# Kernel optimization log

Hardware: AMD Instinct MI355X
Metric: run time of the kernel (lower is better)

Reference implementation:

```python
import jax, jax.numpy as jnp
import numpy as np
from jax import lax

N_NODES = 10000
N_EDGES = 320000


def setup_inputs() -> dict:
    key = jax.random.key(0)
    ks = jax.random.split(key, 7)
    B, H, N, F = 4, 24, N_NODES, 32
    hid = 64
    x = jax.random.normal(ks[0], (B, H, N, F), dtype=jnp.float32)
    mask = jax.random.uniform(ks[1], (B, H), dtype=jnp.float32)
    edge_index = jax.random.randint(ks[2], (2, N_EDGES), 0, N, dtype=jnp.int32)
    W1 = jax.random.normal(ks[3], (F + 1, hid), dtype=jnp.float32) * (1.0 / np.sqrt(F + 1))
    b1 = jax.random.normal(ks[4], (hid,), dtype=jnp.float32) * 0.02
    W2 = jax.random.normal(ks[5], (hid, F), dtype=jnp.float32) * (1.0 / np.sqrt(hid))
    b2 = jax.random.normal(ks[6], (F,), dtype=jnp.float32) * 0.02
    return {"x": x, "mask": mask, "edge_index": edge_index,
            "W1": W1, "b1": b1, "W2": W2, "b2": b2}


def _gcn_norm(edge_index, num_nodes):
    # PyG GCNConv default: add self loops, symmetric normalization.
    loops = jnp.arange(num_nodes, dtype=edge_index.dtype)
    src = jnp.concatenate([edge_index[0], loops])
    dst = jnp.concatenate([edge_index[1], loops])
    deg = jax.ops.segment_sum(jnp.ones_like(dst, dtype=jnp.float32), dst,
                              num_segments=num_nodes)
    dinv = jnp.where(deg > 0, lax.rsqrt(jnp.maximum(deg, 1e-12)), 0.0)
    norm = dinv[src] * dinv[dst]  # [E']
    return src, dst, norm


def reference(x, mask, edge_index, W1, b1, W2, b2):
    B, H, N, F = x.shape
    src, dst, norm = _gcn_norm(edge_index, N)

    def gcn(h, W, b):
        # h: [B, N, Fin] -> lin, then normalized neighbor aggregation, then bias
        hw = h @ W                                   # [B, N, Fout]
        msg = hw[:, src, :].transpose(1, 0, 2)       # [E', B, Fout]
        msg = msg * norm[:, None, None]
        agg = jax.ops.segment_sum(msg, dst, num_segments=N)  # [N, B, Fout]
        return agg.transpose(1, 0, 2) + b

    def per_hour(carry, inp):
        xh, mh = inp                                 # xh: [B, N, F], mh: [B]
        mc = jnp.broadcast_to(mh[:, None, None], (B, N, 1))
        h = jnp.concatenate([xh, mc], axis=-1)       # [B, N, F+1]
        out = jnp.tanh(gcn(gcn(h, W1, b1), W2, b2))  # [B, N, F]
        return carry, out

    _, outs = lax.scan(per_hour, None,
                       (x.transpose(1, 0, 2, 3), mask.T))  # [H, B, N, F]
    return outs.transpose(1, 0, 2, 3)                     # [B, H, N, F]
```

## Files before the change

### kernel.cpp

```cpp
#include <hip/hip_runtime.h>
#include <hip/hip_fp16.h>

#define NN 10000
#define FF 32
#define PG 4
#define NGRP 24

typedef __attribute__((ext_vector_type(2))) float f32x2;

__device__ __forceinline__ unsigned short f2h(float f){
  union { unsigned short s; _Float16 h; } c; c.h = (_Float16)f; return c.s;
}

__device__ __forceinline__ void fmix2(float& ax, float& ay, float w, unsigned h){
  asm("v_fma_mix_f32 %0, %2, %3, %0 op_sel_hi:[0,1,0]\n\t"
      "v_fma_mix_f32 %1, %2, %3, %1 op_sel:[0,1,0] op_sel_hi:[0,1,0]"
      : "+v"(ax), "+v"(ay) : "v"(w), "v"(h));
}

__device__ __forceinline__ void pkfma(f32x2& acc, f32x2 w, f32x2 x){
  asm("v_pk_fma_f32 %0, %1, %2, %0" : "+v"(acc) : "s"(w), "v"(x));
}

__global__ void k_count(const int* __restrict__ dst, int* __restrict__ cnt,
                        int2* __restrict__ csr, int csrcap, int E){
  int e = blockIdx.x * 256 + threadIdx.x;
  if (e >= E) return;
  csr[e] = make_int2(0, 0);
  int e2 = e + E;
  if (e2 < csrcap) csr[e2] = make_int2(0, 0);
  atomicAdd(&cnt[dst[e]], 1);
}

__global__ __launch_bounds__(1024) void k_scan(const int* __restrict__ cnt,
                                               int* __restrict__ off,
                                               float* __restrict__ dinv,
                                               const float* __restrict__ W1,
                                               const float* __restrict__ W2,
                                               const float* __restrict__ b1,
                                               float* __restrict__ W12,
                                               float* __restrict__ bb){
  __shared__ int wsum[16];
  __shared__ int carry;
  int tid = threadIdx.x, lane = tid & 63, wv = tid >> 6;
  if (tid == 0) carry = 0;
  __syncthreads();
  for (int base = 0; base < NN; base += 1024){
    int i = base + tid;
    int c = (i < NN) ? cnt[i] : 0;
    int v = (c + 3) & ~3;
    int s = v;
    #pragma unroll
    for (int o = 1; o < 64; o <<= 1){
      int t = __shfl_up(s, o, 64);
      if (lane >= o) s += t;
    }
    if (lane == 63) wsum[wv] = s;
    __syncthreads();
    if (tid == 0){
      int a = carry;
      #pragma unroll
      for (int k = 0; k < 16; ++k){ int t = wsum[k]; wsum[k] = a; a += t; }
      carry = a;
    }
    __syncthreads();
    if (i < NN){
      off[i]  = wsum[wv] + s - v;
      dinv[i] = rsqrtf((float)(c + 1));
    }
    __syncthreads();
  }
  if (tid == 0) off[NN] = carry;
  for (int idx = tid; idx < 33 * 32; idx += 1024){
    int k = idx >> 5, j = idx & 31;
    float s = 0.f;
    for (int m = 0; m < 64; ++m) s += W1[k * 64 + m] * W2[m * 32 + j];
    W12[idx] = s;
  }
  if (tid < 32){
    int j = tid;
    float s = 0.f;
    for (int m = 0; m < 64; ++m) s += b1[m] * W2[m * 32 + j];
    bb[j] = s;
  }
}

__global__ void k_scatter(const int* __restrict__ ei, const int* __restrict__ off,
                          int* __restrict__ cur, const float* __restrict__ dinv,
                          int2* __restrict__ csr, float* __restrict__ srow, int E){
  int e = blockIdx.x * 256 + threadIdx.x;
  if (e >= E) return;
  int s = ei[e], d = ei[E + e];
  float ds = dinv[s];
  int pos = off[d] + atomicAdd(&cur[d], 1);
  csr[pos] = make_int2(s << 8, __float_as_int(ds));
  atomicAdd(&srow[d], ds);
}

__global__ __launch_bounds__(256) void k_gemm1(const float* __restrict__ x,
    const float* __restrict__ mask, const float* __restrict__ W12,
    unsigned* __restrict__ hw){
  const int pg = blockIdx.y;
  const int n  = blockIdx.x * 256 + threadIdx.x;
  const int grp = pg >> 2, p = pg & 3;
  const float mv = mask[pg];
  const f32x2* Wp = (const f32x2*)W12;
  f32x2 acc[16];
  #pragma unroll
  for (int qf = 0; qf < 16; ++qf){
    f32x2 w = Wp[32 * 16 + qf];
    acc[qf].x = mv * w.x; acc[qf].y = mv * w.y;
  }
  if (n >= NN) return;
  const float4* xp = (const float4*)(x + (size_t)pg * (NN * FF) + (size_t)n * FF);
  float xv[32];
  #pragma unroll
  for (int i = 0; i < 8; ++i){
    float4 v = xp[i];
    xv[4*i]   = v.x; xv[4*i+1] = v.y;
    xv[4*i+2] = v.z; xv[4*i+3] = v.w;
  }
  #pragma unroll
  for (int k = 0; k < 32; ++k){
    f32x2 xk2; xk2.x = xv[k]; xk2.y = xv[k];
    #pragma unroll
    for (int qf = 0; qf < 16; ++qf) pkfma(acc[qf], Wp[k * 16 + qf], xk2);
  }
  unsigned* hwg = hw + (size_t)grp * (NN * 64) + ((size_t)n << 6) + (p << 4);
  #pragma unroll
  for (int j = 0; j < 4; ++j){
    uint4 u;
    u.x = (unsigned)f2h(acc[4*j+0].x) | ((unsigned)f2h(acc[4*j+0].y) << 16);
    u.y = (unsigned)f2h(acc[4*j+1].x) | ((unsigned)f2h(acc[4*j+1].y) << 16);
    u.z = (unsigned)f2h(acc[4*j+2].x) | ((unsigned)f2h(acc[4*j+2].y) << 16);
    u.w = (unsigned)f2h(acc[4*j+3].x) | ((unsigned)f2h(acc[4*j+3].y) << 16);
    ((uint4*)hwg)[j] = u;
  }
}

__device__ __forceinline__ void map_block(int bx, int& grp, int& chunk){
  int r  = bx / 5000;
  int w8 = bx % 5000;
  grp   = r * 8 + (w8 & 7);
  chunk = w8 >> 3;
}

__device__ __forceinline__ void agg_edges(int e0, int e1,
    const int2* __restrict__ csr, const char* __restrict__ Vb, int loff,
    float& ax, float& ay){
  int nq = (e1 - e0) >> 2;
  if (nq <= 0) return;
  const int4* c4 = (const int4*)(csr + e0);
  const int qlast = nq - 1;
  int4 cA, dA, cB, dB, cC, dC, cD, dD;
  int4 cA2, dA2, cB2, dB2, cC2, dC2, cD2, dD2;
  unsigned rA0,rA1,rA2,rA3, rB0,rB1,rB2,rB3;
  unsigned rC0,rC1,rC2,rC3, rD0,rD1,rD2,rD3;
  {
    int i1 = 1<=qlast?1:qlast, i2 = 2<=qlast?2:qlast, i3 = 3<=qlast?3:qlast;
    cA = c4[0];      dA = c4[1];
    cB = c4[2*i1];   dB = c4[2*i1+1];
    cC = c4[2*i2];   dC = c4[2*i2+1];
    cD = c4[2*i3];   dD = c4[2*i3+1];
    int i4 = 4<=qlast?4:qlast, i5 = 5<=qlast?5:qlast;
    int i6 = 6<=qlast?6:qlast, i7 = 7<=qlast?7:qlast;
    cA2 = c4[2*i4];  dA2 = c4[2*i4+1];
    cB2 = c4[2*i5];  dB2 = c4[2*i5+1];
    cC2 = c4[2*i6];  dC2 = c4[2*i6+1];
    cD2 = c4[2*i7];  dD2 = c4[2*i7+1];
    rA0 = *(const unsigned*)(Vb + (unsigned)(cA.x + loff));
    rA1 = *(const unsigned*)(Vb + (unsigned)(cA.z + loff));
    rA2 = *(const unsigned*)(Vb + (unsigned)(dA.x + loff));
    rA3 = *(const unsigned*)(Vb + (unsigned)(dA.z + loff));
    rB0 = *(const unsigned*)(Vb + (unsigned)(cB.x + loff));
    rB1 = *(const unsigned*)(Vb + (unsigned)(cB.z + loff));
    rB2 = *(const unsigned*)(Vb + (unsigned)(dB.x + loff));
    rB3 = *(const unsigned*)(Vb + (unsigned)(dB.z + loff));
    rC0 = *(const unsigned*)(Vb + (unsigned)(cC.x + loff));
    rC1 = *(const unsigned*)(Vb + (unsigned)(cC.z + loff));
    rC2 = *(const unsigned*)(Vb + (unsigned)(dC.x + loff));
    rC3 = *(const unsigned*)(Vb + (unsigned)(dC.z + loff));
    rD0 = *(const unsigned*)(Vb + (unsigned)(cD.x + loff));
    rD1 = *(const unsigned*)(Vb + (unsigned)(cD.z + loff));
    rD2 = *(const unsigned*)(Vb + (unsigned)(dD.x + loff));
    rD3 = *(const unsigned*)(Vb + (unsigned)(dD.z + loff));
  }
  int q = 0;
  #define AGG_STEP(cX, dX, cX2, dX2, r0, r1, r2, r3, LEAD)              \
    do {                                                                \
      fmix2(ax, ay, __int_as_float(cX.y), r0);                          \
      fmix2(ax, ay, __int_as_float(cX.w), r1);                          \
      fmix2(ax, ay, __int_as_float(dX.y), r2);                          \
      fmix2(ax, ay, __int_as_float(dX.w), r3);                          \
      r0 = *(const unsigned*)(Vb + (unsigned)(cX2.x + loff));           \
      r1 = *(const unsigned*)(Vb + (unsigned)(cX2.z + loff));           \
      r2 = *(const unsigned*)(Vb + (unsigned)(dX2.x + loff));           \
      r3 = *(const unsigned*)(Vb + (unsigned)(dX2.z + loff));           \
      cX = cX2; dX = dX2;                                               \
      int ii = q + (LEAD); ii = ii <= qlast ? ii : qlast;               \
      cX2 = c4[2*ii]; dX2 = c4[2*ii+1];                                 \
    } while (0)
  for (; q + 3 < nq; q += 4){
    AGG_STEP(cA,dA,cA2,dA2, rA0,rA1,rA2,rA3, 8);
    AGG_STEP(cB,dB,cB2,dB2, rB0,rB1,rB2,rB3, 9);
    AGG_STEP(cC,dC,cC2,dC2, rC0,rC1,rC2,rC3, 10);
    AGG_STEP(cD,dD,cD2,dD2, rD0,rD1,rD2,rD3, 11);
  }
  #undef AGG_STEP
  int rem = nq - q;
  if (rem > 0){
    fmix2(ax, ay, __int_as_float(cA.y), rA0);
    fmix2(ax, ay, __int_as_float(cA.w), rA1);
    fmix2(ax, ay, __int_as_float(dA.y), rA2);
    fmix2(ax, ay, __int_as_float(dA.w), rA3);
  }
  if (rem > 1){
    fmix2(ax, ay, __int_as_float(cB.y), rB0);
    fmix2(ax, ay, __int_as_float(cB.w), rB1);
    fmix2(ax, ay, __int_as_float(dB.y), rB2);
    fmix2(ax, ay, __int_as_float(dB.w), rB3);
  }
  if (rem > 2){
    fmix2(ax, ay, __int_as_float(cC.y), rC0);
    fmix2(ax, ay, __int_as_float(cC.w), rC1);
    fmix2(ax, ay, __int_as_float(dC.y), rC2);
    fmix2(ax, ay, __int_as_float(dC.w), rC3);
  }
}

__global__ __launch_bounds__(256) void k_agg1(const int* __restrict__ off,
    const int2* __restrict__ csr, const float* __restrict__ dinv,
    const unsigned int* __restrict__ V, unsigned int* __restrict__ T){
  int grp, chunk; map_block(blockIdx.x, grp, chunk);
  int tid = threadIdx.x;
  int l = tid & 63;
  int wv = __builtin_amdgcn_readfirstlane(tid) >> 6;
  const char* Vb = (const char*)(V + (size_t)grp * (NN * 64));
  unsigned int* Tg = T + (size_t)grp * (NN * 64);
  int loff = l * 4;
  for (int it = 0; it < 4; ++it){
    int n = chunk * 16 + wv * 4 + it;
    float din = dinv[n];
    int e0 = off[n], e1 = off[n + 1];
    unsigned sv = *(const unsigned*)(Vb + (unsigned)((n << 8) + loff));
    union { unsigned u; _Float16 h[2]; } cv; cv.u = sv;
    float ax = din * (float)cv.h[0];
    float ay = din * (float)cv.h[1];
    agg_edges(e0, e1, csr, Vb, loff, ax, ay);
    Tg[((size_t)n << 6) + l] =
        (unsigned)f2h(din * ax) | ((unsigned)f2h(din * ay) << 16);
  }
}

__global__ __launch_bounds__(256) void k_agg2(const int* __restrict__ off,
    const int2* __restrict__ csr, const float* __restrict__ dinv,
    const float* __restrict__ srow, const float* __restrict__ bb,
    const float* __restrict__ b2, const unsigned int* __restrict__ V,
    float* __restrict__ out){
  int grp, chunk; map_block(blockIdx.x, grp, chunk);
  int tid = threadIdx.x;
  int l = tid & 63;
  int wv = __builtin_amdgcn_readfirstlane(tid) >> 6;
  int p = l >> 4, fi = l & 15;
  const char* Vb = (const char*)(V + (size_t)grp * (NN * 64));
  int pg = grp * PG + p;
  float2 bbq = ((const float2*)bb)[fi];
  float2 b2q = ((const float2*)b2)[fi];
  float* outp = out + (size_t)pg * (NN * FF);
  int loff = l * 4;
  for (int it = 0; it < 4; ++it){
    int n = chunk * 16 + wv * 4 + it;
    float din = dinv[n];
    int e0 = off[n], e1 = off[n + 1];
    unsigned sv = *(const unsigned*)(Vb + (unsigned)((n << 8) + loff));
    union { unsigned u; _Float16 h[2]; } cv; cv.u = sv;
    float ax = din * (float)cv.h[0];
    float ay = din * (float)cv.h[1];
    agg_edges(e0, e1, csr, Vb, loff, ax, ay);
    float sr = din * (din + srow[n]);
    float2 o;
    o.x = tanhf(din * ax + sr * bbq.x + b2q.x);
    o.y = tanhf(din * ay + sr * bbq.y + b2q.y);
    ((float2*)(outp + (size_t)n * FF))[fi] = o;
  }
}

extern "C" void kernel_launch(void* const* d_in, const int* in_sizes, int n_in,
                              void* d_out, int out_size, void* d_ws, size_t ws_size,
                              hipStream_t stream){
  const float* x    = (const float*)d_in[0];
  const float* mask = (const float*)d_in[1];
  const int*   ei   = (const int*)d_in[2];
  const float* W1   = (const float*)d_in[3];
  const float* b1   = (const float*)d_in[4];
  const float* W2   = (const float*)d_in[5];
  const float* b2   = (const float*)d_in[6];
  float* out = (float*)d_out;
  const int E = in_sizes[2] / 2;
  const int CSRCAP = E + 3 * NN + 64;

  char* wsp = (char*)d_ws;
  auto alloc = [&](size_t bytes) -> char* {
    char* p = wsp; wsp += (bytes + 255) & ~(size_t)255; return p;
  };
  int*   cnt  = (int*)  alloc((size_t)NN * 4);
  int*   off  = (int*)  alloc((size_t)(NN + 1) * 4);
  int*   cur  = (int*)  alloc((size_t)NN * 4);
  float* srow = (float*)alloc((size_t)NN * 4);
  float* dinv = (float*)alloc((size_t)NN * 4);
  float* W12  = (float*)alloc(33 * 32 * 4);
  float* bbv  = (float*)alloc(32 * 4);
  int2*  csr  = (int2*) alloc((size_t)CSRCAP * 8);
  const size_t per_group = (size_t)NN * 64 * 4;
  unsigned int* hw = (unsigned int*)alloc((size_t)NGRP * per_group);
  unsigned int* t1 = (unsigned int*)alloc((size_t)NGRP * per_group);

  size_t zspan = (size_t)((char*)dinv - (char*)cnt);
  hipMemsetAsync(cnt, 0, zspan, stream);
  k_count  <<<(E + 255) / 256, 256, 0, stream>>>(ei + E, cnt, csr, CSRCAP, E);
  k_scan   <<<1, 1024, 0, stream>>>(cnt, off, dinv, W1, W2, b1, W12, bbv);
  k_scatter<<<(E + 255) / 256, 256, 0, stream>>>(ei, off, cur, dinv, csr, srow, E);

  k_gemm1<<<dim3(40, 96), 256, 0, stream>>>(x, mask, W12, hw);
  k_agg1 <<<15000, 256, 0, stream>>>(off, csr, dinv, hw, t1);
  k_agg2 <<<15000, 256, 0, stream>>>(off, csr, dinv, srow, bbv, b2, t1, out);
}
```

Measured before the change: 513.4 us.

## Pack CSR edges into 32-bit words and replace serial scan with atomic allocation

```diff
diff --git a/kernel.cpp b/kernel.cpp
--- a/kernel.cpp
+++ b/kernel.cpp
@@ -12,10 +12,15 @@
   union { unsigned short s; _Float16 h; } c; c.h = (_Float16)f; return c.s;
 }
 
-__device__ __forceinline__ void fmix2(float& ax, float& ay, float w, unsigned h){
+__device__ __forceinline__ void fmix2p(float& ax, float& ay, unsigned wpk, unsigned h){
+  asm("v_fma_mix_f32 %0, %2, %3, %0 op_sel_hi:[1,1,0]\n\t"
+      "v_fma_mix_f32 %1, %2, %3, %1 op_sel:[0,1,0] op_sel_hi:[1,1,0]"
+      : "+v"(ax), "+v"(ay) : "s"(wpk), "v"(h));
+}
+__device__ __forceinline__ void fmix2s(float& ax, float& ay, float w, unsigned h){
   asm("v_fma_mix_f32 %0, %2, %3, %0 op_sel_hi:[0,1,0]\n\t"
       "v_fma_mix_f32 %1, %2, %3, %1 op_sel:[0,1,0] op_sel_hi:[0,1,0]"
-      : "+v"(ax), "+v"(ay) : "v"(w), "v"(h));
+      : "+v"(ax), "+v"(ay) : "s"(w), "v"(h));
 }
 
 __device__ __forceinline__ void pkfma(f32x2& acc, f32x2 w, f32x2 x){
@@ -23,77 +28,54 @@
 }
 
 __global__ void k_count(const int* __restrict__ dst, int* __restrict__ cnt,
-                        int2* __restrict__ csr, int csrcap, int E){
+                        unsigned* __restrict__ csr, int csrcap, int E){
   int e = blockIdx.x * 256 + threadIdx.x;
   if (e >= E) return;
-  csr[e] = make_int2(0, 0);
+  csr[e] = 0u;
   int e2 = e + E;
-  if (e2 < csrcap) csr[e2] = make_int2(0, 0);
+  if (e2 < csrcap) csr[e2] = 0u;
   atomicAdd(&cnt[dst[e]], 1);
 }
 
-__global__ __launch_bounds__(1024) void k_scan(const int* __restrict__ cnt,
-                                               int* __restrict__ off,
-                                               float* __restrict__ dinv,
-                                               const float* __restrict__ W1,
-                                               const float* __restrict__ W2,
-                                               const float* __restrict__ b1,
-                                               float* __restrict__ W12,
-                                               float* __restrict__ bb){
-  __shared__ int wsum[16];
-  __shared__ int carry;
-  int tid = threadIdx.x, lane = tid & 63, wv = tid >> 6;
-  if (tid == 0) carry = 0;
-  __syncthreads();
-  for (int base = 0; base < NN; base += 1024){
-    int i = base + tid;
-    int c = (i < NN) ? cnt[i] : 0;
-    int v = (c + 3) & ~3;
-    int s = v;
-    #pragma unroll
-    for (int o = 1; o < 64; o <<= 1){
-      int t = __shfl_up(s, o, 64);
-      if (lane >= o) s += t;
-    }
-    if (lane == 63) wsum[wv] = s;
-    __syncthreads();
-    if (tid == 0){
-      int a = carry;
-      #pragma unroll
-      for (int k = 0; k < 16; ++k){ int t = wsum[k]; wsum[k] = a; a += t; }
-      carry = a;
-    }
-    __syncthreads();
+__global__ __launch_bounds__(256) void k_prep(const int* __restrict__ cnt,
+    int2* __restrict__ oe, float* __restrict__ dinv, int* __restrict__ gtop,
+    const float* __restrict__ W1, const float* __restrict__ W2,
+    const float* __restrict__ b1, float* __restrict__ W12, float* __restrict__ bb){
+  int bx = blockIdx.x, tid = threadIdx.x;
+  if (bx < 40){
+    int i = bx * 256 + tid;
     if (i < NN){
-      off[i]  = wsum[wv] + s - v;
+      int c = cnt[i];
+      int pad = (c + 3) & ~3;
+      int start = atomicAdd(gtop, pad);
+      oe[i] = make_int2(start, start + pad);
       dinv[i] = rsqrtf((float)(c + 1));
     }
-    __syncthreads();
-  }
-  if (tid == 0) off[NN] = carry;
-  for (int idx = tid; idx < 33 * 32; idx += 1024){
-    int k = idx >> 5, j = idx & 31;
-    float s = 0.f;
-    for (int m = 0; m < 64; ++m) s += W1[k * 64 + m] * W2[m * 32 + j];
-    W12[idx] = s;
-  }
-  if (tid < 32){
-    int j = tid;
-    float s = 0.f;
-    for (int m = 0; m < 64; ++m) s += b1[m] * W2[m * 32 + j];
-    bb[j] = s;
-  }
-}
-
-__global__ void k_scatter(const int* __restrict__ ei, const int* __restrict__ off,
+  } else {
+    int j = (bx - 40) * 256 + tid;
+    if (j < 33 * 32){
+      int k = j >> 5, c = j & 31;
+      float s = 0.f;
+      for (int m = 0; m < 64; ++m) s += W1[k * 64 + m] * W2[m * 32 + c];
+      W12[j] = s;
+    } else if (j < 33 * 32 + 32){
+      int c = j - 33 * 32;
+      float s = 0.f;
+      for (int m = 0; m < 64; ++m) s += b1[m] * W2[m * 32 + c];
+      bb[c] = s;
+    }
+  }
+}
+
+__global__ void k_scatter(const int* __restrict__ ei, const int2* __restrict__ oe,
                           int* __restrict__ cur, const float* __restrict__ dinv,
-                          int2* __restrict__ csr, float* __restrict__ srow, int E){
+                          unsigned* __restrict__ csr, float* __restrict__ srow, int E){
   int e = blockIdx.x * 256 + threadIdx.x;
   if (e >= E) return;
   int s = ei[e], d = ei[E + e];
   float ds = dinv[s];
-  int pos = off[d] + atomicAdd(&cur[d], 1);
-  csr[pos] = make_int2(s << 8, __float_as_int(ds));
+  int pos = oe[d].x + atomicAdd(&cur[d], 1);
+  csr[pos] = ((unsigned)s << 16) | (unsigned)f2h(ds);
   atomicAdd(&srow[d], ds);
 }
 
@@ -145,91 +127,74 @@
   chunk = w8 >> 3;
 }
 
+#define ROWB(w) ((((unsigned)(w)) >> 8) & 0xFFFF00u)
 __device__ __forceinline__ void agg_edges(int e0, int e1,
-    const int2* __restrict__ csr, const char* __restrict__ Vb, int loff,
+    const unsigned* __restrict__ csr, const char* __restrict__ Vb, int loff,
     float& ax, float& ay){
   int nq = (e1 - e0) >> 2;
   if (nq <= 0) return;
   const int4* c4 = (const int4*)(csr + e0);
   const int qlast = nq - 1;
-  int4 cA, dA, cB, dB, cC, dC, cD, dD;
-  int4 cA2, dA2, cB2, dB2, cC2, dC2, cD2, dD2;
+  #define VLD(w) (*(const unsigned*)(Vb + (unsigned)(ROWB(w) + loff)))
+  int4 cA, cB, cC, cD;
+  int4 cA2, cB2, cC2, cD2;
   unsigned rA0,rA1,rA2,rA3, rB0,rB1,rB2,rB3;
   unsigned rC0,rC1,rC2,rC3, rD0,rD1,rD2,rD3;
   {
     int i1 = 1<=qlast?1:qlast, i2 = 2<=qlast?2:qlast, i3 = 3<=qlast?3:qlast;
-    cA = c4[0];      dA = c4[1];
-    cB = c4[2*i1];   dB = c4[2*i1+1];
-    cC = c4[2*i2];   dC = c4[2*i2+1];
-    cD = c4[2*i3];   dD = c4[2*i3+1];
+    cA = c4[0]; cB = c4[i1]; cC = c4[i2]; cD = c4[i3];
     int i4 = 4<=qlast?4:qlast, i5 = 5<=qlast?5:qlast;
     int i6 = 6<=qlast?6:qlast, i7 = 7<=qlast?7:qlast;
-    cA2 = c4[2*i4];  dA2 = c4[2*i4+1];
-    cB2 = c4[2*i5];  dB2 = c4[2*i5+1];
-    cC2 = c4[2*i6];  dC2 = c4[2*i6+1];
-    cD2 = c4[2*i7];  dD2 = c4[2*i7+1];
-    rA0 = *(const unsigned*)(Vb + (unsigned)(cA.x + loff));
-    rA1 = *(const unsigned*)(Vb + (unsigned)(cA.z + loff));
-    rA2 = *(const unsigned*)(Vb + (unsigned)(dA.x + loff));
-    rA3 = *(const unsigned*)(Vb + (unsigned)(dA.z + loff));
-    rB0 = *(const unsigned*)(Vb + (unsigned)(cB.x + loff));
-    rB1 = *(const unsigned*)(Vb + (unsigned)(cB.z + loff));
-    rB2 = *(const unsigned*)(Vb + (unsigned)(dB.x + loff));
-    rB3 = *(const unsigned*)(Vb + (unsigned)(dB.z + loff));
-    rC0 = *(const unsigned*)(Vb + (unsigned)(cC.x + loff));
-    rC1 = *(const unsigned*)(Vb + (unsigned)(cC.z + loff));
-    rC2 = *(const unsigned*)(Vb + (unsigned)(dC.x + loff));
-    rC3 = *(const unsigned*)(Vb + (unsigned)(dC.z + loff));
-    rD0 = *(const unsigned*)(Vb + (unsigned)(cD.x + loff));
-    rD1 = *(const unsigned*)(Vb + (unsigned)(cD.z + loff));
-    rD2 = *(const unsigned*)(Vb + (unsigned)(dD.x + loff));
-    rD3 = *(const unsigned*)(Vb + (unsigned)(dD.z + loff));
+    cA2 = c4[i4]; cB2 = c4[i5]; cC2 = c4[i6]; cD2 = c4[i7];
+    rA0 = VLD(cA.x); rA1 = VLD(cA.y); rA2 = VLD(cA.z); rA3 = VLD(cA.w);
+    rB0 = VLD(cB.x); rB1 = VLD(cB.y); rB2 = VLD(cB.z); rB3 = VLD(cB.w);
+    rC0 = VLD(cC.x); rC1 = VLD(cC.y); rC2 = VLD(cC.z); rC3 = VLD(cC.w);
+    rD0 = VLD(cD.x); rD1 = VLD(cD.y); rD2 = VLD(cD.z); rD3 = VLD(cD.w);
   }
   int q = 0;
-  #define AGG_STEP(cX, dX, cX2, dX2, r0, r1, r2, r3, LEAD)              \
+  #define AGG_STEP(cX, cX2, r0, r1, r2, r3, LEAD)                       \
     do {                                                                \
-      fmix2(ax, ay, __int_as_float(cX.y), r0);                          \
-      fmix2(ax, ay, __int_as_float(cX.w), r1);                          \
-      fmix2(ax, ay, __int_as_float(dX.y), r2);                          \
-      fmix2(ax, ay, __int_as_float(dX.w), r3);                          \
-      r0 = *(const unsigned*)(Vb + (unsigned)(cX2.x + loff));           \
-      r1 = *(const unsigned*)(Vb + (unsigned)(cX2.z + loff));           \
-      r2 = *(const unsigned*)(Vb + (unsigned)(dX2.x + loff));           \
-      r3 = *(const unsigned*)(Vb + (unsigned)(dX2.z + loff));           \
-      cX = cX2; dX = dX2;                                               \
+      fmix2p(ax, ay, (unsigned)cX.x, r0);                               \
+      fmix2p(ax, ay, (unsigned)cX.y, r1);                               \
+      fmix2p(ax, ay, (unsigned)cX.z, r2);                               \
+      fmix2p(ax, ay, (unsigned)cX.w, r3);                               \
+      r0 = VLD(cX2.x); r1 = VLD(cX2.y);                                 \
+      r2 = VLD(cX2.z); r3 = VLD(cX2.w);                                 \
+      cX = cX2;                                                         \
       int ii = q + (LEAD); ii = ii <= qlast ? ii : qlast;               \
-      cX2 = c4[2*ii]; dX2 = c4[2*ii+1];                                 \
+      cX2 = c4[ii];                                                     \
     } while (0)
   for (; q + 3 < nq; q += 4){
-    AGG_STEP(cA,dA,cA2,dA2, rA0,rA1,rA2,rA3, 8);
-    AGG_STEP(cB,dB,cB2,dB2, rB0,rB1,rB2,rB3, 9);
-    AGG_STEP(cC,dC,cC2,dC2, rC0,rC1,rC2,rC3, 10);
-    AGG_STEP(cD,dD,cD2,dD2, rD0,rD1,rD2,rD3, 11);
+    AGG_STEP(cA, cA2, rA0,rA1,rA2,rA3, 8);
+    AGG_STEP(cB, cB2, rB0,rB1,rB2,rB3, 9);
+    AGG_STEP(cC, cC2, rC0,rC1,rC2,rC3, 10);
+    AGG_STEP(cD, cD2, rD0,rD1,rD2,rD3, 11);
   }
   #undef AGG_STEP
+  #undef VLD
   int rem = nq - q;
   if (rem > 0){
-    fmix2(ax, ay, __int_as_float(cA.y), rA0);
-    fmix2(ax, ay, __int_as_float(cA.w), rA1);
-    fmix2(ax, ay, __int_as_float(dA.y), rA2);
-    fmix2(ax, ay, __int_as_float(dA.w), rA3);
+    fmix2p(ax, ay, (unsigned)cA.x, rA0);
+    fmix2p(ax, ay, (unsigned)cA.y, rA1);
+    fmix2p(ax, ay, (unsigned)cA.z, rA2);
+    fmix2p(ax, ay, (unsigned)cA.w, rA3);
   }
   if (rem > 1){
-    fmix2(ax, ay, __int_as_float(cB.y), rB0);
-    fmix2(ax, ay, __int_as_float(cB.w), rB1);
-    fmix2(ax, ay, __int_as_float(dB.y), rB2);
-    fmix2(ax, ay, __int_as_float(dB.w), rB3);
+    fmix2p(ax, ay, (unsigned)cB.x, rB0);
+    fmix2p(ax, ay, (unsigned)cB.y, rB1);
+    fmix2p(ax, ay, (unsigned)cB.z, rB2);
+    fmix2p(ax, ay, (unsigned)cB.w, rB3);
   }
   if (rem > 2){
-    fmix2(ax, ay, __int_as_float(cC.y), rC0);
-    fmix2(ax, ay, __int_as_float(cC.w), rC1);
-    fmix2(ax, ay, __int_as_float(dC.y), rC2);
-    fmix2(ax, ay, __int_as_float(dC.w), rC3);
-  }
-}
-
-__global__ __launch_bounds__(256) void k_agg1(const int* __restrict__ off,
-    const int2* __restrict__ csr, const float* __restrict__ dinv,
+    fmix2p(ax, ay, (unsigned)cC.x, rC0);
+    fmix2p(ax, ay, (unsigned)cC.y, rC1);
+    fmix2p(ax, ay, (unsigned)cC.z, rC2);
+    fmix2p(ax, ay, (unsigned)cC.w, rC3);
+  }
+}
+
+__global__ __launch_bounds__(256) void k_agg1(const int2* __restrict__ oe,
+    const unsigned* __restrict__ csr, const float* __restrict__ dinv,
     const unsigned int* __restrict__ V, unsigned int* __restrict__ T){
   int grp, chunk; map_block(blockIdx.x, grp, chunk);
   int tid = threadIdx.x;
@@ -241,19 +206,18 @@
   for (int it = 0; it < 4; ++it){
     int n = chunk * 16 + wv * 4 + it;
     float din = dinv[n];
-    int e0 = off[n], e1 = off[n + 1];
+    int2 ee = oe[n];
     unsigned sv = *(const unsigned*)(Vb + (unsigned)((n << 8) + loff));
-    union { unsigned u; _Float16 h[2]; } cv; cv.u = sv;
-    float ax = din * (float)cv.h[0];
-    float ay = din * (float)cv.h[1];
-    agg_edges(e0, e1, csr, Vb, loff, ax, ay);
+    float ax = 0.f, ay = 0.f;
+    fmix2s(ax, ay, din, sv);
+    agg_edges(ee.x, ee.y, csr, Vb, loff, ax, ay);
     Tg[((size_t)n << 6) + l] =
         (unsigned)f2h(din * ax) | ((unsigned)f2h(din * ay) << 16);
   }
 }
 
-__global__ __launch_bounds__(256) void k_agg2(const int* __restrict__ off,
-    const int2* __restrict__ csr, const float* __restrict__ dinv,
+__global__ __launch_bounds__(256) void k_agg2(const int2* __restrict__ oe,
+    const unsigned* __restrict__ csr, const float* __restrict__ dinv,
     const float* __restrict__ srow, const float* __restrict__ bb,
     const float* __restrict__ b2, const unsigned int* __restrict__ V,
     float* __restrict__ out){
@@ -271,12 +235,11 @@
   for (int it = 0; it < 4; ++it){
     int n = chunk * 16 + wv * 4 + it;
     float din = dinv[n];
-    int e0 = off[n], e1 = off[n + 1];
+    int2 ee = oe[n];
     unsigned sv = *(const unsigned*)(Vb + (unsigned)((n << 8) + loff));
-    union { unsigned u; _Float16 h[2]; } cv; cv.u = sv;
-    float ax = din * (float)cv.h[0];
-    float ay = din * (float)cv.h[1];
-    agg_edges(e0, e1, csr, Vb, loff, ax, ay);
+    float ax = 0.f, ay = 0.f;
+    fmix2s(ax, ay, din, sv);
+    agg_edges(ee.x, ee.y, csr, Vb, loff, ax, ay);
     float sr = din * (din + srow[n]);
     float2 o;
     o.x = tanhf(din * ax + sr * bbq.x + b2q.x);
@@ -304,13 +267,14 @@
     char* p = wsp; wsp += (bytes + 255) & ~(size_t)255; return p;
   };
   int*   cnt  = (int*)  alloc((size_t)NN * 4);
-  int*   off  = (int*)  alloc((size_t)(NN + 1) * 4);
   int*   cur  = (int*)  alloc((size_t)NN * 4);
   float* srow = (float*)alloc((size_t)NN * 4);
+  int*   gtop = (int*)  alloc(256);
   float* dinv = (float*)alloc((size_t)NN * 4);
+  int2*  oe   = (int2*) alloc((size_t)NN * 8);
   float* W12  = (float*)alloc(33 * 32 * 4);
   float* bbv  = (float*)alloc(32 * 4);
-  int2*  csr  = (int2*) alloc((size_t)CSRCAP * 8);
+  unsigned* csr = (unsigned*)alloc((size_t)CSRCAP * 4);
   const size_t per_group = (size_t)NN * 64 * 4;
   unsigned int* hw = (unsigned int*)alloc((size_t)NGRP * per_group);
   unsigned int* t1 = (unsigned int*)alloc((size_t)NGRP * per_group);
@@ -318,10 +282,10 @@
   size_t zspan = (size_t)((char*)dinv - (char*)cnt);
   hipMemsetAsync(cnt, 0, zspan, stream);
   k_count  <<<(E + 255) / 256, 256, 0, stream>>>(ei + E, cnt, csr, CSRCAP, E);
-  k_scan   <<<1, 1024, 0, stream>>>(cnt, off, dinv, W1, W2, b1, W12, bbv);
-  k_scatter<<<(E + 255) / 256, 256, 0, stream>>>(ei, off, cur, dinv, csr, srow, E);
+  k_prep   <<<45, 256, 0, stream>>>(cnt, oe, dinv, gtop, W1, W2, b1, W12, bbv);
+  k_scatter<<<(E + 255) / 256, 256, 0, stream>>>(ei, oe, cur, dinv, csr, srow, E);
 
   k_gemm1<<<dim3(40, 96), 256, 0, stream>>>(x, mask, W12, hw);
-  k_agg1 <<<15000, 256, 0, stream>>>(off, csr, dinv, hw, t1);
-  k_agg2 <<<15000, 256, 0, stream>>>(off, csr, dinv, srow, bbv, b2, t1, out);
-}
+  k_agg1 <<<15000, 256, 0, stream>>>(oe, csr, dinv, hw, t1);
+  k_agg2 <<<15000, 256, 0, stream>>>(oe, csr, dinv, srow, bbv, b2, t1, out);
+}
```

Result: faster. 495.7 us (-3.4%).
